# Kernel optimization log

Hardware: AMD Instinct MI355X
Metric: run time of the kernel (lower is better)

The kernel has to match this reference:

```python
import jax, jax.numpy as jnp
import numpy as np

B, N, D, H, L, M = 2, 1024, 512, 8, 4, 256
DFF = 4 * D
LN_EPS = 1e-5


def layer_norm(x, g, b):
    mu = x.mean(-1, keepdims=True)
    var = x.var(-1, keepdims=True)
    return (x - mu) * jax.lax.rsqrt(var + LN_EPS) * g + b


def setup_inputs() -> dict:
    key = jax.random.key(0)
    ks = iter(jax.random.split(key, 32))
    s = 0.02
    inp = {
        "phi": jax.random.normal(next(ks), (B, N, D), jnp.float32),
        "coords": jax.random.normal(next(ks), (B, N, 3), jnp.float32),
        # CoordinateEncoding: Gaussian Fourier modes (init_std=0.05) + linear
        "modes": 0.05 * jax.random.normal(next(ks), (M, 3), jnp.float32),
        "We": s * jax.random.normal(next(ks), (2 * M, D), jnp.float32),
        "be": jnp.zeros((D,), jnp.float32),
        # per-block attention params, stacked over L blocks
        "wq": s * jax.random.normal(next(ks), (L, D, D), jnp.float32),
        "bq": jnp.zeros((L, D), jnp.float32),
        "wk": s * jax.random.normal(next(ks), (L, D, D), jnp.float32),
        "bk": jnp.zeros((L, D), jnp.float32),
        "wv": s * jax.random.normal(next(ks), (L, D, D), jnp.float32),
        "bv": jnp.zeros((L, D), jnp.float32),
        "wo": s * jax.random.normal(next(ks), (L, D, D), jnp.float32),
        "bo": jnp.zeros((L, D), jnp.float32),
        "temp": jnp.ones((L, H), jnp.float32),  # per-head distance temperature
        "ln1_g": jnp.ones((L, D), jnp.float32),
        "ln1_b": jnp.zeros((L, D), jnp.float32),
        "ln2_g": jnp.ones((L, D), jnp.float32),
        "ln2_b": jnp.zeros((L, D), jnp.float32),
        "w1": s * jax.random.normal(next(ks), (L, D, DFF), jnp.float32),
        "b1": jnp.zeros((L, DFF), jnp.float32),
        "w2": s * jax.random.normal(next(ks), (L, DFF, D), jnp.float32),
        "b2": jnp.zeros((L, D), jnp.float32),
        "fng": jnp.ones((D,), jnp.float32),
        "fnb": jnp.zeros((D,), jnp.float32),
    }
    return inp


def reference(phi, coords, modes, We, be, wq, bq, wk, bk, wv, bv, wo, bo, temp,
              ln1_g, ln1_b, ln2_g, ln2_b, w1, b1, w2, b2, fng, fnb):
    dh = D // H
    # coordinate encoding (random Fourier features)
    phase = jnp.einsum('bnc,mc->bnm', coords, modes)            # [B,N,M]
    feats = jnp.concatenate([jnp.cos(phase), jnp.sin(phase)], -1)  # [B,N,2M]
    x = phi + feats @ We + be
    # pairwise distances with epsilon shift, std-scaled per sample
    diff = coords[:, :, None, :] - (coords + 1e-5)[:, None, :, :]
    d = jnp.sqrt(jnp.sum(diff * diff, -1))                      # [B,N,N]
    d = d / jnp.std(d, axis=(-2, -1), keepdims=True, ddof=1)
    scale = 1.0 / np.sqrt(dh)
    for l in range(L):
        y = layer_norm(x, ln1_g[l], ln1_b[l])
        q = (y @ wq[l] + bq[l]).reshape(B, N, H, dh)
        k = (y @ wk[l] + bk[l]).reshape(B, N, H, dh)
        v = (y @ wv[l] + bv[l]).reshape(B, N, H, dh)
        scores = jnp.einsum('bihd,bjhd->bhij', q, k) * scale
        scores = scores - jax.nn.softplus(temp[l])[None, :, None, None] * d[:, None]
        a = jax.nn.softmax(scores, axis=-1)                     # [B,H,N,N]
        o = jnp.einsum('bhij,bjhd->bihd', a, v).reshape(B, N, D)
        x = x + o @ wo[l] + bo[l]
        z = layer_norm(x, ln2_g[l], ln2_b[l])
        h = jax.nn.gelu(z @ w1[l] + b1[l], approximate=False)
        x = x + h @ w2[l] + b2[l]
    return layer_norm(x, fng, fnb)
```

## Files before the change

kernel.cpp:

```cpp
#include <hip/hip_runtime.h>
#include <hip/hip_bf16.h>
#include <math.h>

#define BATCH 2
#define NTOK 1024
#define DMODEL 512
#define NHEAD 8
#define DH 64
#define NLAYER 4
#define MMODES 256
#define DFFN 2048

typedef unsigned short u16;
typedef __attribute__((ext_vector_type(4))) float f4;
typedef __attribute__((ext_vector_type(8))) short b8;

__device__ __forceinline__ float bf2f(u16 u) { return __uint_as_float(((unsigned)u) << 16); }
__device__ __forceinline__ u16 f2b(float x) {
    unsigned u = __float_as_uint(x);
    return (u16)((u + 0x7FFF + ((u >> 16) & 1)) >> 16);
}
__device__ __forceinline__ float ldx(const void* p, size_t i, int f32) {
    return f32 ? ((const float*)p)[i] : bf2f(((const u16*)p)[i]);
}
__device__ __forceinline__ void async_ld16(const u16* g, u16* l) {
    __builtin_amdgcn_global_load_lds((const __attribute__((address_space(1))) void*)g,
                                     (__attribute__((address_space(3))) void*)l, 16, 0, 0);
}

__global__ __launch_bounds__(256) void detect_kernel(const void* __restrict__ probe,
                                                     int* __restrict__ flag) {
    const u16* u = (const u16*)probe;
    int big = 0, zer = 0;
    for (int t = threadIdx.x; t < 768; t += 256) {
        u16 w = u[2 * t];
        int e = (w >> 7) & 0xFF;
        if (e >= 137) big++;
        if (w == 0) zer++;
    }
    __shared__ int sb, sz;
    if (threadIdx.x == 0) { sb = 0; sz = 0; }
    __syncthreads();
    atomicAdd(&sb, big);
    atomicAdd(&sz, zer);
    __syncthreads();
    if (threadIdx.x == 0) flag[0] = (sb >= 64 || sz >= 700) ? 1 : 0;
}

__global__ __launch_bounds__(256) void cvt_all_kernel(const void* __restrict__ phi,
                                                      const void* __restrict__ coords,
                                                      float* __restrict__ xf,
                                                      float* __restrict__ cf,
                                                      const int* __restrict__ fl) {
    int f = fl[0];
    int i = blockIdx.x * 256 + threadIdx.x;
    if (i < BATCH * NTOK * DMODEL) xf[i] = ldx(phi, i, f);
    if (i < BATCH * NTOK * 3) cf[i] = ldx(coords, i, f);
}

#define OB_BE 0
#define OB_BQKV 512
#define OB_BO 6656
#define OB_B1 8704
#define OB_B2 16896
#define OB_TEMP 18944
#define OB_L1G 18976
#define OB_L1B 21024
#define OB_L2G 23072
#define OB_L2B 25120
#define OB_FNG 27168
#define OB_FNB 27680
#define OB_MODES 28192
#define OB_TOTAL 28960
__global__ __launch_bounds__(256) void pack_params(
    const void* be_, const void* bq_, const void* bk_, const void* bv_,
    const void* bo_, const void* b1_, const void* b2_, const void* temp_,
    const void* l1g_, const void* l1b_, const void* l2g_, const void* l2b_,
    const void* fng_, const void* fnb_, const void* modes_,
    float* __restrict__ out, const int* __restrict__ fl) {
    int f = fl[0];
    for (int idx = blockIdx.x * 256 + threadIdx.x; idx < OB_TOTAL; idx += gridDim.x * 256) {
        float v;
        int i = idx;
        if (i < 512) v = ldx(be_, i, f);
        else if ((i -= 512) < 6144) {
            int l = i / 1536, r = i - l * 1536;
            v = (r < 512) ? ldx(bq_, (size_t)l * 512 + r, f)
              : (r < 1024) ? ldx(bk_, (size_t)l * 512 + r - 512, f)
              : ldx(bv_, (size_t)l * 512 + r - 1024, f);
        }
        else if ((i -= 6144) < 2048) v = ldx(bo_, i, f);
        else if ((i -= 2048) < 8192) v = ldx(b1_, i, f);
        else if ((i -= 8192) < 2048) v = ldx(b2_, i, f);
        else if ((i -= 2048) < 32)   v = ldx(temp_, i, f);
        else if ((i -= 32) < 2048)   v = ldx(l1g_, i, f);
        else if ((i -= 2048) < 2048) v = ldx(l1b_, i, f);
        else if ((i -= 2048) < 2048) v = ldx(l2g_, i, f);
        else if ((i -= 2048) < 2048) v = ldx(l2b_, i, f);
        else if ((i -= 2048) < 512)  v = ldx(fng_, i, f);
        else if ((i -= 512) < 512)   v = ldx(fnb_, i, f);
        else { i -= 512; v = ldx(modes_, i, f); }
        out[idx] = v;
    }
}

__device__ __forceinline__ void tr_body(const void* src, size_t sbase, u16* dst,
                                        size_t dbase, int R, int C, int dstRowOff, int f) {
    __shared__ float t[32][33];
    int c0 = blockIdx.x * 32, r0 = blockIdx.y * 32;
    int tx = threadIdx.x & 31, ty8 = threadIdx.x >> 5;
#pragma unroll
    for (int rr = 0; rr < 4; rr++) {
        int r = r0 + ty8 + rr * 8;
        t[ty8 + rr * 8][tx] = ldx(src, sbase + (size_t)r * C + c0 + tx, f);
    }
    __syncthreads();
#pragma unroll
    for (int rr = 0; rr < 4; rr++) {
        int c = c0 + ty8 + rr * 8;
        dst[dbase + (size_t)(dstRowOff + c) * R + r0 + tx] = f2b(t[tx][ty8 + rr * 8]);
    }
}
__global__ __launch_bounds__(256) void tr_qkv(const void* wq_, const void* wk_,
                                              const void* wv_, u16* dst,
                                              const int* __restrict__ fl) {
    int z = blockIdx.z, l = z / 3, mat = z - l * 3;
    const void* s = (mat == 0) ? wq_ : (mat == 1) ? wk_ : wv_;
    tr_body(s, (size_t)l * 512 * 512, dst, (size_t)l * 1536 * 512, 512, 512, mat * 512, fl[0]);
}
__global__ __launch_bounds__(256) void tr_woWe(const void* wo_, const void* We_,
                                               u16* woT, u16* WeT,
                                               const int* __restrict__ fl) {
    int z = blockIdx.z;
    if (z < 4) tr_body(wo_, (size_t)z * 512 * 512, woT, (size_t)z * 512 * 512, 512, 512, 0, fl[0]);
    else       tr_body(We_, 0, WeT, 0, 512, 512, 0, fl[0]);
}
__global__ __launch_bounds__(256) void tr_gen(const void* src, u16* dst, int R, int C,
                                              const int* __restrict__ fl) {
    int z = blockIdx.z;
    tr_body(src, (size_t)z * R * C, dst, (size_t)z * R * C, R, C, 0, fl[0]);
}

__global__ __launch_bounds__(256) void feats_kernel(const float* __restrict__ cf,
                                                    const float* __restrict__ modesF,
                                                    u16* __restrict__ ff) {
    int row = blockIdx.x, m = threadIdx.x;
    float cx = cf[row * 3 + 0], cy = cf[row * 3 + 1], cz = cf[row * 3 + 2];
    float ph = cx * modesF[m * 3 + 0] + cy * modesF[m * 3 + 1] + cz * modesF[m * 3 + 2];
    ff[(size_t)row * 512 + m] = f2b(cosf(ph));
    ff[(size_t)row * 512 + MMODES + m] = f2b(sinf(ph));
}

__global__ __launch_bounds__(256) void dstat_kernel(const float* __restrict__ cf,
                                                    float* __restrict__ part,
                                                    u16* __restrict__ dist) {
    int b = blockIdx.x >> 10, i = blockIdx.x & 1023;
    const float* cb = cf + (size_t)b * NTOK * 3;
    float xi = cb[i * 3], yi = cb[i * 3 + 1], zi = cb[i * 3 + 2];
    float ls = 0.f, ls2 = 0.f;
    for (int j = threadIdx.x; j < NTOK; j += 256) {
        float dx = xi - (cb[j * 3] + 1e-5f);
        float dy = yi - (cb[j * 3 + 1] + 1e-5f);
        float dz = zi - (cb[j * 3 + 2] + 1e-5f);
        float d = sqrtf(dx * dx + dy * dy + dz * dz);
        if (dist) dist[(((size_t)(b * NTOK + i)) << 10) + j] = f2b(d);
        ls += d; ls2 += d * d;
    }
    for (int off = 32; off; off >>= 1) {
        ls += __shfl_down(ls, off);
        ls2 += __shfl_down(ls2, off);
    }
    __shared__ float rs[4], rs2[4];
    int wid = threadIdx.x >> 6;
    if ((threadIdx.x & 63) == 0) { rs[wid] = ls; rs2[wid] = ls2; }
    __syncthreads();
    if (threadIdx.x == 0) {
        part[blockIdx.x] = rs[0] + rs[1] + rs[2] + rs[3];
        part[2048 + blockIdx.x] = rs2[0] + rs2[1] + rs2[2] + rs2[3];
    }
}
__global__ __launch_bounds__(256) void dreduce_kernel(const float* __restrict__ part,
                                                      float* __restrict__ inv_std) {
    int b = blockIdx.x;
    double s = 0.0, s2 = 0.0;
    for (int t = threadIdx.x; t < NTOK; t += 256) {
        s += (double)part[b * NTOK + t];
        s2 += (double)part[2048 + b * NTOK + t];
    }
    for (int off = 32; off; off >>= 1) {
        s += __shfl_down(s, off);
        s2 += __shfl_down(s2, off);
    }
    __shared__ double ds[4], ds2[4];
    int wid = threadIdx.x >> 6;
    if ((threadIdx.x & 63) == 0) { ds[wid] = s; ds2[wid] = s2; }
    __syncthreads();
    if (threadIdx.x == 0) {
        double S = ds[0] + ds[1] + ds[2] + ds[3];
        double S2 = ds2[0] + ds2[1] + ds2[2] + ds2[3];
        double n = (double)NTOK * (double)NTOK;
        double mean = S / n;
        double var = (S2 - n * mean * mean) / (n - 1.0);
        inv_std[b] = (float)(1.0 / sqrt(var));
    }
}

__global__ __launch_bounds__(256) void ln_bf_kernel(const float* __restrict__ x,
                                                    const float* __restrict__ gp,
                                                    const float* __restrict__ bp,
                                                    u16* __restrict__ y) {
    int row = blockIdx.x, tid = threadIdx.x;
    const float* xr = x + (size_t)row * DMODEL;
    float v0 = xr[tid], v1 = xr[tid + 256];
    float s = v0 + v1, s2 = v0 * v0 + v1 * v1;
    for (int off = 32; off; off >>= 1) {
        s += __shfl_down(s, off);
        s2 += __shfl_down(s2, off);
    }
    __shared__ float ls[4], ls2[4];
    int wid = tid >> 6;
    if ((tid & 63) == 0) { ls[wid] = s; ls2[wid] = s2; }
    __syncthreads();
    s = ls[0] + ls[1] + ls[2] + ls[3];
    s2 = ls2[0] + ls2[1] + ls2[2] + ls2[3];
    float mean = s * (1.0f / DMODEL);
    float var = s2 * (1.0f / DMODEL) - mean * mean;
    float r = rsqrtf(var + 1e-5f);
    y[(size_t)row * DMODEL + tid] = f2b((v0 - mean) * r * gp[tid] + bp[tid]);
    y[(size_t)row * DMODEL + tid + 256] = f2b((v1 - mean) * r * gp[tid + 256] + bp[tid + 256]);
}
__global__ __launch_bounds__(256) void ln_out_kernel(const float* __restrict__ x,
                                                     const float* __restrict__ gp,
                                                     const float* __restrict__ bp,
                                                     void* __restrict__ out,
                                                     const int* __restrict__ fl) {
    int f = fl[0];
    int row = blockIdx.x, tid = threadIdx.x;
    const float* xr = x + (size_t)row * DMODEL;
    float v0 = xr[tid], v1 = xr[tid + 256];
    float s = v0 + v1, s2 = v0 * v0 + v1 * v1;
    for (int off = 32; off; off >>= 1) {
        s += __shfl_down(s, off);
        s2 += __shfl_down(s2, off);
    }
    __shared__ float ls[4], ls2[4];
    int wid = tid >> 6;
    if ((tid & 63) == 0) { ls[wid] = s; ls2[wid] = s2; }
    __syncthreads();
    s = ls[0] + ls[1] + ls[2] + ls[3];
    s2 = ls2[0] + ls2[1] + ls2[2] + ls2[3];
    float mean = s * (1.0f / DMODEL);
    float var = s2 * (1.0f / DMODEL) - mean * mean;
    float r = rsqrtf(var + 1e-5f);
    float o0 = (v0 - mean) * r * gp[tid] + bp[tid];
    float o1 = (v1 - mean) * r * gp[tid + 256] + bp[tid + 256];
    size_t i0 = (size_t)row * DMODEL + tid;
    if (f) { ((float*)out)[i0] = o0; ((float*)out)[i0 + 256] = o1; }
    else   { ((u16*)out)[i0] = f2b(o0); ((u16*)out)[i0 + 256] = f2b(o1); }
}

template <int FM, int FN, int ACT, int RES, int OUTBF>
__global__ __launch_bounds__(256) void gemm_mfma(const u16* __restrict__ A,
                                                 const u16* __restrict__ BT,
                                                 const float* __restrict__ bias,
                                                 const float* __restrict__ res,
                                                 void* __restrict__ Cp,
                                                 int M, int N, int K) {
    constexpr int BM = 32 * FM, BN = 32 * FN;
    constexpr int PA = BM / 64, PB = BN / 64;
    __shared__ u16 As[BM * 32];
    __shared__ u16 Bs[BN * 32];
    const int m0 = blockIdx.y * BM, n0 = blockIdx.x * BN;
    const int tid = threadIdx.x, lane = tid & 63, wid = tid >> 6;
    const int wm = (wid >> 1) * (16 * FM), wn = (wid & 1) * (16 * FN);
    const int quad = lane >> 4, low = lane & 15;
    const int srow = tid >> 2, scol = (tid & 3) * 8;
    f4 acc[FM][FN] = {};
    for (int k0 = 0; k0 < K; k0 += 32) {
#pragma unroll
        for (int p = 0; p < PA; p++)
            async_ld16(A + (size_t)(m0 + p * 64 + srow) * K + k0 + scol,
                       As + p * 2048 + wid * 512);
#pragma unroll
        for (int p = 0; p < PB; p++)
            async_ld16(BT + (size_t)(n0 + p * 64 + srow) * K + k0 + scol,
                       Bs + p * 2048 + wid * 512);
        __syncthreads();
        b8 af[FM], bfr[FN];
#pragma unroll
        for (int i = 0; i < FM; i++)
            af[i] = *(const b8*)(As + (wm + i * 16 + low) * 32 + quad * 8);
#pragma unroll
        for (int j = 0; j < FN; j++)
            bfr[j] = *(const b8*)(Bs + (wn + j * 16 + low) * 32 + quad * 8);
#pragma unroll
        for (int i = 0; i < FM; i++)
#pragma unroll
            for (int j = 0; j < FN; j++)
                acc[i][j] = __builtin_amdgcn_mfma_f32_16x16x32_bf16(af[i], bfr[j], acc[i][j], 0, 0, 0);
        __syncthreads();
    }
#pragma unroll
    for (int i = 0; i < FM; i++) {
#pragma unroll
        for (int j = 0; j < FN; j++) {
            int gn = n0 + wn + j * 16 + low;
            float bv = bias[gn];
#pragma unroll
            for (int r = 0; r < 4; r++) {
                int gm = m0 + wm + i * 16 + quad * 4 + r;
                float v = acc[i][j][r] + bv;
                if (ACT) v = 0.5f * v * (1.0f + erff(v * 0.70710678f));
                if (RES) v += res[(size_t)gm * N + gn];
                if (OUTBF) ((u16*)Cp)[(size_t)gm * N + gn] = f2b(v);
                else       ((float*)Cp)[(size_t)gm * N + gn] = v;
            }
        }
    }
}

template <int USE_DIST>
__global__ __launch_bounds__(256) void attn_mfma(const u16* __restrict__ qkv,
                                                 const float* __restrict__ cf,
                                                 const float* __restrict__ inv_std,
                                                 const float* __restrict__ tempF, int l,
                                                 const u16* __restrict__ dist,
                                                 u16* __restrict__ o) {
    const int it = blockIdx.x, h = blockIdx.y, b = blockIdx.z;
    const int i0 = it * 32, tid = threadIdx.x;
    const int lane = tid & 63, wid = tid >> 6;
    const int g = wid >> 1, p = wid & 1;
    const int quad = lane >> 4, low = lane & 15;
    __shared__ u16 Ks[2][64][72];
    __shared__ u16 Vs[2][64][72];
    __shared__ u16 Ps[4][16][72];
    __shared__ float s_ci[32][3];
    __shared__ float s_cj[2][64][3];
    const size_t rbase = (size_t)b * NTOK;
    b8 qf0, qf1;
    {
        const u16* qp = qkv + (rbase + i0 + g * 16 + low) * 1536 + h * 64;
        qf0 = *(const b8*)(qp + quad * 8);
        qf1 = *(const b8*)(qp + 32 + quad * 8);
    }
    if (!USE_DIST && tid < 32) {
        s_ci[tid][0] = cf[(rbase + i0 + tid) * 3 + 0];
        s_ci[tid][1] = cf[(rbase + i0 + tid) * 3 + 1];
        s_ci[tid][2] = cf[(rbase + i0 + tid) * 3 + 2];
    }
    float t0 = tempF[l * 8 + h];
    float spw = (fmaxf(t0, 0.f) + log1pf(__expf(-fabsf(t0)))) * inv_std[b];
    float mold[4] = {-1e30f, -1e30f, -1e30f, -1e30f};
    float lsum[4] = {0.f, 0.f, 0.f, 0.f};
    f4 oacc[4] = {};
    __syncthreads();
    float cqx[4], cqy[4], cqz[4];
    const u16* drow[4];
#pragma unroll
    for (int r = 0; r < 4; r++) {
        int ii = g * 16 + quad * 4 + r;
        if (USE_DIST) drow[r] = dist + ((rbase + i0 + ii) << 10);
        else { cqx[r] = s_ci[ii][0]; cqy[r] = s_ci[ii][1]; cqz[r] = s_ci[ii][2]; }
    }
    for (int t = 0; t < 8; t++) {
        __syncthreads();
#pragma unroll
        for (int tt = 0; tt < 2; tt++) {
            int j0s = (t * 2 + tt) * 64;
            int j = tid >> 2, dc = (tid & 3) * 16;
            const u16* kp = qkv + (rbase + j0s + j) * 1536 + 512 + h * 64 + dc;
            *(uint4*)&Ks[tt][j][dc] = *(const uint4*)kp;
            *(uint4*)&Ks[tt][j][dc + 8] = *(const uint4*)(kp + 8);
            const u16* vp = qkv + (rbase + j0s + lane) * 1536 + 1024 + h * 64 + wid * 16;
            uint4 v0 = *(const uint4*)vp, v1 = *(const uint4*)(vp + 8);
            const u16* ve = (const u16*)&v0;
            const u16* ve2 = (const u16*)&v1;
#pragma unroll
            for (int e = 0; e < 8; e++) {
                Vs[tt][wid * 16 + e][lane] = ve[e];
                Vs[tt][wid * 16 + 8 + e][lane] = ve2[e];
            }
            if (!USE_DIST && tid < 64) {
                s_cj[tt][tid][0] = cf[(rbase + j0s + tid) * 3 + 0] + 1e-5f;
                s_cj[tt][tid][1] = cf[(rbase + j0s + tid) * 3 + 1] + 1e-5f;
                s_cj[tt][tid][2] = cf[(rbase + j0s + tid) * 3 + 2] + 1e-5f;
            }
        }
        __syncthreads();
        const int j0 = (t * 2 + p) * 64;
        f4 sacc[4] = {};
#pragma unroll
        for (int jb = 0; jb < 4; jb++) {
            b8 bk0 = *(const b8*)&Ks[p][jb * 16 + low][quad * 8];
            b8 bk1 = *(const b8*)&Ks[p][jb * 16 + low][32 + quad * 8];
            sacc[jb] = __builtin_amdgcn_mfma_f32_16x16x32_bf16(qf0, bk0, sacc[jb], 0, 0, 0);
            sacc[jb] = __builtin_amdgcn_mfma_f32_16x16x32_bf16(qf1, bk1, sacc[jb], 0, 0, 0);
        }
        float sv[4][4];
#pragma unroll
        for (int jb = 0; jb < 4; jb++) {
            int j = jb * 16 + low;
            if (USE_DIST) {
#pragma unroll
                for (int r = 0; r < 4; r++)
                    sv[jb][r] = sacc[jb][r] * 0.125f - spw * bf2f(drow[r][j0 + j]);
            } else {
                float cjx = s_cj[p][j][0], cjy = s_cj[p][j][1], cjz = s_cj[p][j][2];
#pragma unroll
                for (int r = 0; r < 4; r++) {
                    float dx = cqx[r] - cjx, dy = cqy[r] - cjy, dz = cqz[r] - cjz;
                    sv[jb][r] = sacc[jb][r] * 0.125f - spw * sqrtf(dx * dx + dy * dy + dz * dz);
                }
            }
        }
        float alpha[4];
#pragma unroll
        for (int r = 0; r < 4; r++) {
            float mx = fmaxf(fmaxf(sv[0][r], sv[1][r]), fmaxf(sv[2][r], sv[3][r]));
            mx = fmaxf(mx, __shfl_xor(mx, 1));
            mx = fmaxf(mx, __shfl_xor(mx, 2));
            mx = fmaxf(mx, __shfl_xor(mx, 4));
            mx = fmaxf(mx, __shfl_xor(mx, 8));
            float mn = fmaxf(mold[r], mx);
            alpha[r] = __expf(mold[r] - mn);
            mold[r] = mn;
            float ps = 0.f;
#pragma unroll
            for (int jb = 0; jb < 4; jb++) {
                float pp = __expf(sv[jb][r] - mn);
                Ps[wid][quad * 4 + r][jb * 16 + low] = f2b(pp);
                ps += pp;
            }
            ps += __shfl_xor(ps, 1);
            ps += __shfl_xor(ps, 2);
            ps += __shfl_xor(ps, 4);
            ps += __shfl_xor(ps, 8);
            lsum[r] = lsum[r] * alpha[r] + ps;
        }
#pragma unroll
        for (int db = 0; db < 4; db++)
#pragma unroll
            for (int r = 0; r < 4; r++) oacc[db][r] *= alpha[r];
        b8 ap0 = *(const b8*)&Ps[wid][low][quad * 8];
        b8 ap1 = *(const b8*)&Ps[wid][low][32 + quad * 8];
#pragma unroll
        for (int db = 0; db < 4; db++) {
            b8 bv0 = *(const b8*)&Vs[p][db * 16 + low][quad * 8];
            b8 bv1 = *(const b8*)&Vs[p][db * 16 + low][32 + quad * 8];
            oacc[db] = __builtin_amdgcn_mfma_f32_16x16x32_bf16(ap0, bv0, oacc[db], 0, 0, 0);
            oacc[db] = __builtin_amdgcn_mfma_f32_16x16x32_bf16(ap1, bv1, oacc[db], 0, 0, 0);
        }
    }
    __syncthreads();
    float* scr = (float*)&Ks[0][0][0];
    float* Og = scr + g * 1088;
    float* Ml = Og + 1024;
    if (p == 1) {
#pragma unroll
        for (int db = 0; db < 4; db++)
#pragma unroll
            for (int r = 0; r < 4; r++)
                Og[(quad * 4 + r) * 64 + db * 16 + low] = oacc[db][r];
        if (low == 0) {
#pragma unroll
            for (int r = 0; r < 4; r++) {
                Ml[quad * 4 + r] = mold[r];
                Ml[16 + quad * 4 + r] = lsum[r];
            }
        }
    }
    __syncthreads();
    if (p == 0) {
#pragma unroll
        for (int r = 0; r < 4; r++) {
            int row = quad * 4 + r;
            float m1 = Ml[row], l1 = Ml[16 + row];
            float mm = fmaxf(mold[r], m1);
            float a0 = __expf(mold[r] - mm), a1 = __expf(m1 - mm);
            float rl = 1.f / (lsum[r] * a0 + l1 * a1);
            u16* op = o + (rbase + i0 + g * 16 + row) * 512 + h * 64 + low;
#pragma unroll
            for (int db = 0; db < 4; db++) {
                float v = oacc[db][r] * a0 + Og[row * 64 + db * 16 + low] * a1;
                op[db * 16] = f2b(v * rl);
            }
        }
    }
}

extern "C" void kernel_launch(void* const* d_in, const int* in_sizes, int n_in,
                              void* d_out, int out_size, void* d_ws, size_t ws_size,
                              hipStream_t stream) {
    const void* phi    = d_in[0];
    const void* coords = d_in[1];
    const void* modes  = d_in[2];
    const void* We     = d_in[3];
    const void* be     = d_in[4];
    const void* wq     = d_in[5];
    const void* bq     = d_in[6];
    const void* wk     = d_in[7];
    const void* bk     = d_in[8];
    const void* wv     = d_in[9];
    const void* bv     = d_in[10];
    const void* wo     = d_in[11];
    const void* bo     = d_in[12];
    const void* temp   = d_in[13];
    const void* ln1g   = d_in[14];
    const void* ln1b   = d_in[15];
    const void* ln2g   = d_in[16];
    const void* ln2b   = d_in[17];
    const void* w1     = d_in[18];
    const void* b1     = d_in[19];
    const void* w2     = d_in[20];
    const void* b2     = d_in[21];
    const void* fng    = d_in[22];
    const void* fnb    = d_in[23];

    const int R = BATCH * NTOK;
    char* ws = (char*)d_ws;
    const size_t MB = 1u << 20;
    float* xf   = (float*)(ws);
    u16*  yf    = (u16*)(ws + 4 * MB);
    u16*  of    = (u16*)(ws + 6 * MB);
    u16*  pool  = (u16*)(ws + 8 * MB);
    u16*  ff    = pool;
    u16*  qkvb  = pool;
    u16*  hf    = pool;
    u16*  WeT   = (u16*)(ws + 16 * MB);
    u16*  wqkvT = (u16*)(ws + 16 * MB + 512 * 1024);
    u16*  woT   = (u16*)(ws + 22 * MB + 512 * 1024);
    u16*  w1T   = (u16*)(ws + 24 * MB + 512 * 1024);
    u16*  w2T   = (u16*)(ws + 32 * MB + 512 * 1024);
    float* prm  = (float*)(ws + 40 * MB + 512 * 1024);
    float* cf   = (float*)(ws + 41 * MB);
    float* part = (float*)(ws + 41 * MB + 128 * 1024);
    float* inv_std = (float*)(ws + 41 * MB + 192 * 1024);
    int*   flag = (int*)(ws + 41 * MB + 192 * 1024 + 64);
    u16* dist = (ws_size >= (size_t)46 * MB) ? (u16*)(ws + 42 * MB) : nullptr;

    detect_kernel<<<1, 256, 0, stream>>>(wq, flag);
    cvt_all_kernel<<<(R * DMODEL + 255) / 256, 256, 0, stream>>>(phi, coords, xf, cf, flag);
    pack_params<<<32, 256, 0, stream>>>(be, bq, bk, bv, bo, b1, b2, temp,
                                        ln1g, ln1b, ln2g, ln2b, fng, fnb, modes, prm, flag);
    tr_qkv<<<dim3(16, 16, 12), 256, 0, stream>>>(wq, wk, wv, wqkvT, flag);
    tr_woWe<<<dim3(16, 16, 5), 256, 0, stream>>>(wo, We, woT, WeT, flag);
    tr_gen<<<dim3(64, 16, 4), 256, 0, stream>>>(w1, w1T, 512, 2048, flag);
    tr_gen<<<dim3(16, 64, 4), 256, 0, stream>>>(w2, w2T, 2048, 512, flag);

    feats_kernel<<<R, 256, 0, stream>>>(cf, prm + OB_MODES, ff);
    gemm_mfma<2, 2, 0, 1, 0><<<dim3(8, 32), 256, 0, stream>>>(ff, WeT, prm + OB_BE, xf, xf,
                                                              R, DMODEL, DMODEL);
    dstat_kernel<<<R, 256, 0, stream>>>(cf, part, dist);
    dreduce_kernel<<<BATCH, 256, 0, stream>>>(part, inv_std);

    for (int l = 0; l < NLAYER; l++) {
        ln_bf_kernel<<<R, 256, 0, stream>>>(xf, prm + OB_L1G + l * 512, prm + OB_L1B + l * 512, yf);
        gemm_mfma<2, 4, 0, 0, 1><<<dim3(12, 32), 256, 0, stream>>>(
            yf, wqkvT + (size_t)l * 1536 * 512, prm + OB_BQKV + l * 1536, nullptr, qkvb,
            R, 1536, DMODEL);
        if (dist)
            attn_mfma<1><<<dim3(32, NHEAD, BATCH), 256, 0, stream>>>(
                qkvb, cf, inv_std, prm + OB_TEMP, l, dist, of);
        else
            attn_mfma<0><<<dim3(32, NHEAD, BATCH), 256, 0, stream>>>(
                qkvb, cf, inv_std, prm + OB_TEMP, l, nullptr, of);
        gemm_mfma<2, 2, 0, 1, 0><<<dim3(8, 32), 256, 0, stream>>>(
            of, woT + (size_t)l * 512 * 512, prm + OB_BO + l * 512, xf, xf, R, DMODEL, DMODEL);
        ln_bf_kernel<<<R, 256, 0, stream>>>(xf, prm + OB_L2G + l * 512, prm + OB_L2B + l * 512, yf);
        gemm_mfma<4, 4, 1, 0, 1><<<dim3(16, 16), 256, 0, stream>>>(
            yf, w1T + (size_t)l * 2048 * 512, prm + OB_B1 + l * 2048, nullptr, hf,
            R, DFFN, DMODEL);
        gemm_mfma<2, 2, 0, 1, 0><<<dim3(8, 32), 256, 0, stream>>>(
            hf, w2T + (size_t)l * 512 * 2048, prm + OB_B2 + l * 512, xf, xf, R, DMODEL, DFFN);
    }
    ln_out_kernel<<<R, 256, 0, stream>>>(xf, prm + OB_FNG, prm + OB_FNB, d_out, flag);
}
```

Baseline: 599.5 us.

## Widen GEMM K-step, shrink QKV/FFN1 tiles, pre-transpose V for attention

The GEMM now loads two 32-wide K slices per barrier pair, which halves the number of syncs per K sweep at the cost of twice the shared memory. The QKV and FFN1 GEMMs use narrower N tiles so more blocks are launched and the CUs are better filled. A new kernel writes V transposed per head into a workspace buffer, so attention loads V with vectorized 16-byte copies instead of scalar scattered shared-memory stores. The price is one extra kernel launch per layer and an extra read and write of V through global memory.

After: 538.5 us. 10.2% less time.

```diff
diff --git a/kernel.cpp b/kernel.cpp
--- a/kernel.cpp
+++ b/kernel.cpp
@@ -259,6 +259,29 @@
     else   { ((u16*)out)[i0] = f2b(o0); ((u16*)out)[i0 + 256] = f2b(o1); }
 }
 
+__global__ __launch_bounds__(256) void vt_kernel(const u16* __restrict__ qkv,
+                                                 u16* __restrict__ VT) {
+    const int jc = blockIdx.x, h = blockIdx.y, b = blockIdx.z;
+    const int j0 = jc * 64, t = threadIdx.x;
+    __shared__ u16 Ls[64][72];
+    {
+        int j = t >> 2, dc = (t & 3) * 16;
+        const u16* vp = qkv + ((size_t)(b * NTOK + j0 + j)) * 1536 + 1024 + h * 64 + dc;
+        *(uint4*)&Ls[j][dc] = *(const uint4*)vp;
+        *(uint4*)&Ls[j][dc + 8] = *(const uint4*)(vp + 8);
+    }
+    __syncthreads();
+    {
+        int d = t >> 2, jc2 = (t & 3) * 16;
+        u16 tmp[16];
+#pragma unroll
+        for (int e = 0; e < 16; e++) tmp[e] = Ls[jc2 + e][d];
+        u16* dst = VT + ((size_t)(b * 8 + h)) * 65536 + (size_t)d * 1024 + j0 + jc2;
+        *(uint4*)dst = *(uint4*)&tmp[0];
+        *(uint4*)(dst + 8) = *(uint4*)&tmp[8];
+    }
+}
+
 template <int FM, int FN, int ACT, int RES, int OUTBF>
 __global__ __launch_bounds__(256) void gemm_mfma(const u16* __restrict__ A,
                                                  const u16* __restrict__ BT,
@@ -268,36 +291,42 @@
                                                  int M, int N, int K) {
     constexpr int BM = 32 * FM, BN = 32 * FN;
     constexpr int PA = BM / 64, PB = BN / 64;
-    __shared__ u16 As[BM * 32];
-    __shared__ u16 Bs[BN * 32];
+    __shared__ u16 As[2 * BM * 32];
+    __shared__ u16 Bs[2 * BN * 32];
     const int m0 = blockIdx.y * BM, n0 = blockIdx.x * BN;
     const int tid = threadIdx.x, lane = tid & 63, wid = tid >> 6;
     const int wm = (wid >> 1) * (16 * FM), wn = (wid & 1) * (16 * FN);
     const int quad = lane >> 4, low = lane & 15;
     const int srow = tid >> 2, scol = (tid & 3) * 8;
     f4 acc[FM][FN] = {};
-    for (int k0 = 0; k0 < K; k0 += 32) {
-#pragma unroll
-        for (int p = 0; p < PA; p++)
-            async_ld16(A + (size_t)(m0 + p * 64 + srow) * K + k0 + scol,
-                       As + p * 2048 + wid * 512);
-#pragma unroll
-        for (int p = 0; p < PB; p++)
-            async_ld16(BT + (size_t)(n0 + p * 64 + srow) * K + k0 + scol,
-                       Bs + p * 2048 + wid * 512);
+    for (int k0 = 0; k0 < K; k0 += 64) {
+#pragma unroll
+        for (int ks = 0; ks < 2; ks++) {
+#pragma unroll
+            for (int p = 0; p < PA; p++)
+                async_ld16(A + (size_t)(m0 + p * 64 + srow) * K + k0 + ks * 32 + scol,
+                           As + ks * BM * 32 + p * 2048 + wid * 512);
+#pragma unroll
+            for (int p = 0; p < PB; p++)
+                async_ld16(BT + (size_t)(n0 + p * 64 + srow) * K + k0 + ks * 32 + scol,
+                           Bs + ks * BN * 32 + p * 2048 + wid * 512);
+        }
         __syncthreads();
-        b8 af[FM], bfr[FN];
-#pragma unroll
-        for (int i = 0; i < FM; i++)
-            af[i] = *(const b8*)(As + (wm + i * 16 + low) * 32 + quad * 8);
-#pragma unroll
-        for (int j = 0; j < FN; j++)
-            bfr[j] = *(const b8*)(Bs + (wn + j * 16 + low) * 32 + quad * 8);
-#pragma unroll
-        for (int i = 0; i < FM; i++)
+#pragma unroll
+        for (int ks = 0; ks < 2; ks++) {
+            b8 af[FM], bfr[FN];
+#pragma unroll
+            for (int i = 0; i < FM; i++)
+                af[i] = *(const b8*)(As + ks * BM * 32 + (wm + i * 16 + low) * 32 + quad * 8);
 #pragma unroll
             for (int j = 0; j < FN; j++)
-                acc[i][j] = __builtin_amdgcn_mfma_f32_16x16x32_bf16(af[i], bfr[j], acc[i][j], 0, 0, 0);
+                bfr[j] = *(const b8*)(Bs + ks * BN * 32 + (wn + j * 16 + low) * 32 + quad * 8);
+#pragma unroll
+            for (int i = 0; i < FM; i++)
+#pragma unroll
+                for (int j = 0; j < FN; j++)
+                    acc[i][j] = __builtin_amdgcn_mfma_f32_16x16x32_bf16(af[i], bfr[j], acc[i][j], 0, 0, 0);
+        }
         __syncthreads();
     }
 #pragma unroll
@@ -321,6 +350,7 @@
 
 template <int USE_DIST>
 __global__ __launch_bounds__(256) void attn_mfma(const u16* __restrict__ qkv,
+                                                 const u16* __restrict__ VT,
                                                  const float* __restrict__ cf,
                                                  const float* __restrict__ inv_std,
                                                  const float* __restrict__ tempF, int l,
@@ -337,6 +367,7 @@
     __shared__ float s_ci[32][3];
     __shared__ float s_cj[2][64][3];
     const size_t rbase = (size_t)b * NTOK;
+    const u16* VTh = VT + ((size_t)(b * 8 + h)) * 65536;
     b8 qf0, qf1;
     {
         const u16* qp = qkv + (rbase + i0 + g * 16 + low) * 1536 + h * 64;
@@ -371,15 +402,9 @@
             const u16* kp = qkv + (rbase + j0s + j) * 1536 + 512 + h * 64 + dc;
             *(uint4*)&Ks[tt][j][dc] = *(const uint4*)kp;
             *(uint4*)&Ks[tt][j][dc + 8] = *(const uint4*)(kp + 8);
-            const u16* vp = qkv + (rbase + j0s + lane) * 1536 + 1024 + h * 64 + wid * 16;
-            uint4 v0 = *(const uint4*)vp, v1 = *(const uint4*)(vp + 8);
-            const u16* ve = (const u16*)&v0;
-            const u16* ve2 = (const u16*)&v1;
-#pragma unroll
-            for (int e = 0; e < 8; e++) {
-                Vs[tt][wid * 16 + e][lane] = ve[e];
-                Vs[tt][wid * 16 + 8 + e][lane] = ve2[e];
-            }
+            const u16* vp = VTh + (size_t)j * 1024 + j0s + dc;
+            *(uint4*)&Vs[tt][j][dc] = *(const uint4*)vp;
+            *(uint4*)&Vs[tt][j][dc + 8] = *(const uint4*)(vp + 8);
             if (!USE_DIST && tid < 64) {
                 s_cj[tt][tid][0] = cf[(rbase + j0s + tid) * 3 + 0] + 1e-5f;
                 s_cj[tt][tid][1] = cf[(rbase + j0s + tid) * 3 + 1] + 1e-5f;
@@ -525,6 +550,7 @@
     u16*  pool  = (u16*)(ws + 8 * MB);
     u16*  ff    = pool;
     u16*  qkvb  = pool;
+    u16*  VTb   = (u16*)(ws + 14 * MB);
     u16*  hf    = pool;
     u16*  WeT   = (u16*)(ws + 16 * MB);
     u16*  wqkvT = (u16*)(ws + 16 * MB + 512 * 1024);
@@ -555,19 +581,20 @@
 
     for (int l = 0; l < NLAYER; l++) {
         ln_bf_kernel<<<R, 256, 0, stream>>>(xf, prm + OB_L1G + l * 512, prm + OB_L1B + l * 512, yf);
-        gemm_mfma<2, 4, 0, 0, 1><<<dim3(12, 32), 256, 0, stream>>>(
+        gemm_mfma<2, 2, 0, 0, 1><<<dim3(24, 32), 256, 0, stream>>>(
             yf, wqkvT + (size_t)l * 1536 * 512, prm + OB_BQKV + l * 1536, nullptr, qkvb,
             R, 1536, DMODEL);
+        vt_kernel<<<dim3(16, NHEAD, BATCH), 256, 0, stream>>>(qkvb, VTb);
         if (dist)
             attn_mfma<1><<<dim3(32, NHEAD, BATCH), 256, 0, stream>>>(
-                qkvb, cf, inv_std, prm + OB_TEMP, l, dist, of);
+                qkvb, VTb, cf, inv_std, prm + OB_TEMP, l, dist, of);
         else
             attn_mfma<0><<<dim3(32, NHEAD, BATCH), 256, 0, stream>>>(
-                qkvb, cf, inv_std, prm + OB_TEMP, l, nullptr, of);
+                qkvb, VTb, cf, inv_std, prm + OB_TEMP, l, nullptr, of);
         gemm_mfma<2, 2, 0, 1, 0><<<dim3(8, 32), 256, 0, stream>>>(
             of, woT + (size_t)l * 512 * 512, prm + OB_BO + l * 512, xf, xf, R, DMODEL, DMODEL);
         ln_bf_kernel<<<R, 256, 0, stream>>>(xf, prm + OB_L2G + l * 512, prm + OB_L2B + l * 512, yf);
-        gemm_mfma<4, 4, 1, 0, 1><<<dim3(16, 16), 256, 0, stream>>>(
+        gemm_mfma<4, 2, 1, 0, 1><<<dim3(32, 16), 256, 0, stream>>>(
             yf, w1T + (size_t)l * 2048 * 512, prm + OB_B1 + l * 2048, nullptr, hf,
             R, DFFN, DMODEL);
         gemm_mfma<2, 2, 0, 1, 0><<<dim3(8, 32), 256, 0, stream>>>(
```
